# Kernel optimization log

Measured on AMD Instinct MI355X. Metric: run time of the kernel, lower is better.

## Reference

```python
import jax, jax.numpy as jnp
import numpy as np

K_UNF = 11   # unfold kernel = 15 - 4
PAD = 1      # reflection padding for attention branch
KC = 5       # ConvBlock kernel_conv
HEADS = 4
CIN = 64
HD = CIN // HEADS  # head_dim = 16
EPS = 1e-5


def _unfold(x, k):
    # x: [b,C,H,W] -> [b, C*k*k, oh*ow] with torch.nn.Unfold ordering (c, kh, kw)
    b, C, H, W = x.shape
    oh, ow = H - k + 1, W - k + 1
    ih = jnp.arange(oh)[:, None] + jnp.arange(k)[None, :]  # [oh,k]
    iw = jnp.arange(ow)[:, None] + jnp.arange(k)[None, :]  # [ow,k]
    p = x[:, :, ih, :]          # [b,C,oh,k,W]
    p = p[:, :, :, :, iw]       # [b,C,oh,k,ow,k]
    p = p.transpose(0, 1, 3, 5, 2, 4)  # [b,C,kh,kw,oh,ow]
    return p.reshape(b, C * k * k, oh * ow)


def _bn_train(x):
    # BatchNorm2d in training mode, weight=1, bias=0 (fresh module defaults)
    m = x.mean(axis=(0, 2, 3), keepdims=True)
    v = x.var(axis=(0, 2, 3), keepdims=True)
    return (x - m) * jax.lax.rsqrt(v + EPS)


def setup_inputs() -> dict:
    key = jax.random.key(0)
    ks = jax.random.split(key, 6)
    b = 64
    s = 0.02
    x1 = jax.random.normal(ks[0], (b, CIN, 15, 15), jnp.float32)
    Wq = jax.random.normal(ks[1], (CIN, CIN), jnp.float32) * s
    Wk = jax.random.normal(ks[2], (CIN, CIN), jnp.float32) * s
    Wv = jax.random.normal(ks[3], (CIN, CIN), jnp.float32) * s
    fc_w = jax.random.normal(ks[4], (KC * KC, 3 * HEADS), jnp.float32) * s
    convg_w = jax.random.normal(ks[5], (CIN, CIN, 3, 3), jnp.float32) * s
    # dep_conv weight: deterministic one-hot shift kernels per reset_parameters
    dk = np.zeros((KC * KC, KC, KC), np.float32)
    for i in range(KC * KC):
        dk[i, i // KC, i % KC] = 1.0
    dep_w = jnp.asarray(np.broadcast_to(dk[None], (CIN, KC * KC, KC, KC)).copy())
    return {"x1": x1, "Wq": Wq, "Wk": Wk, "Wv": Wv, "fc_w": fc_w,
            "dep_w": dep_w, "convg_w": convg_w}


def reference(x1, Wq, Wk, Wv, fc_w, dep_w, convg_w):
    b, C, h, w = x1.shape  # h=w=15 (i=1 -> size=15)
    size = h
    # 1x1 qkv convs
    q = jnp.einsum('oc,bchw->bohw', Wq, x1)
    k = jnp.einsum('oc,bchw->bohw', Wk, x1)
    v = jnp.einsum('oc,bchw->bohw', Wv, x1)
    # ---- conv branch (ConvBlock) ----
    qkv = jnp.concatenate([t.reshape(b, HEADS, HD, h * w) for t in (q, k, v)], axis=1)  # [b,12,16,225]
    f_all = jnp.einsum('oc,bcds->bods', fc_w, qkv)                 # [b,25,16,225]
    f_conv = f_all.transpose(0, 2, 1, 3).reshape(b, HD * KC * KC, h, w)  # [b,400,15,15]
    out_conv = jax.lax.conv_general_dilated(
        f_conv, dep_w, (1, 1), 'VALID',
        dimension_numbers=('NCHW', 'OIHW', 'NCHW'),
        feature_group_count=HD)                                     # [b,64,11,11]; bias is None
    out_conv = _bn_train(out_conv)
    # ---- attention branch (UnfoldBlock + raw scaled QK^T, no softmax) ----
    def pad_unfold(t):
        tp = jnp.pad(t, ((0, 0), (0, 0), (PAD, PAD), (PAD, PAD)), mode='reflect')
        u = _unfold(tp, K_UNF).transpose(0, 2, 1)  # [b,49,7744]; pos_embed is zeros
        cls = jnp.zeros((b, 1, u.shape[-1]), u.dtype)  # cls token params are zeros
        return jnp.concatenate([cls, u], axis=1)       # [b,50,7744]
    uq, uk, uv = pad_unfold(q), pad_unfold(k), pad_unfold(v)
    N, Cq = uq.shape[1], uq.shape[2]
    query = uq.reshape(b, HEADS, N, Cq // HEADS)  # matches torch reshape semantics
    key_ = uk.reshape(b, HEADS, N, Cq // HEADS)
    val = uv.reshape(b, HEADS, N, Cq // HEADS)
    scaling = float(HD) ** -0.5
    att = jnp.einsum('bhnc,bhmc->bhnm', query, key_) * scaling   # [b,4,50,50]
    out_attn = jnp.einsum('bhnm,bhmc->bhnc', att, val)
    out_attn = out_attn.transpose(0, 2, 1, 3).reshape(b, N, Cq)
    out_attn = out_attn[:, 1, :].reshape(b, CIN, size - 4, size - 4)  # [b,64,11,11]
    out_attn = jax.lax.conv_general_dilated(
        out_attn, convg_w, (1, 1), ((1, 1), (1, 1)),
        dimension_numbers=('NCHW', 'OIHW', 'NCHW'))
    # rate1 and rate2 are filled with 0.5 every forward
    return out_conv * 0.5 + out_attn * 0.5
```

## Files before the change

### kernel.cpp

```cpp
#include <hip/hip_runtime.h>
#include <hip/hip_bf16.h>

#define B 64
#define CIN 64
#define HW 225
#define CQ 7744
#define XS2 116
#define VPS 24

__device__ __forceinline__ int reflect15(int t) {
    return t < 0 ? -t : (t > 14 ? 28 - t : t);
}
__device__ __forceinline__ int refp(int t) { return reflect15(t - 1); }

__global__ __launch_bounds__(512) void qkv_kernel(const float* __restrict__ x1,
                           const float* __restrict__ Wq,
                           const float* __restrict__ Wk,
                           const float* __restrict__ Wv,
                           float* __restrict__ q, float* __restrict__ k, float* __restrict__ v,
                           float* __restrict__ stats) {
    int b = blockIdx.x;
    int t = blockIdx.y;
    int ph = blockIdx.z;
    int tid = threadIdx.x;
    if (b == 0 && t == 0 && ph == 0 && tid < 32) stats[tid] = 0.f;
    const float* W = (t == 0) ? Wq : (t == 1) ? Wk : Wv;
    float* out = (t == 0) ? q : (t == 1) ? k : v;
    __shared__ float xs[CIN * XS2];
    int start = ph ? 113 : 0;
    int count = ph ? 112 : 113;
    const float* xb = x1 + (size_t)b * CIN * HW;
    for (int i = tid; i < CIN * XS2; i += 512) {
        int c = i / XS2, s = i % XS2;
        xs[i] = (s < count) ? xb[c * HW + start + s] : 0.f;
    }
    __syncthreads();
    int og = __builtin_amdgcn_readfirstlane(tid >> 6);
    int lane = tid & 63;
    const float* Wb = W + (size_t)og * 8 * CIN;
    float acc[8][2];
    #pragma unroll
    for (int m = 0; m < 8; ++m) { acc[m][0] = 0.f; acc[m][1] = 0.f; }
    #pragma unroll 4
    for (int c = 0; c < CIN; ++c) {
        float x0 = xs[c * XS2 + lane];
        float x1v = xs[c * XS2 + lane + 64];
        #pragma unroll
        for (int m = 0; m < 8; ++m) {
            float w = Wb[m * CIN + c];
            acc[m][0] += w * x0;
            acc[m][1] += w * x1v;
        }
    }
    float* ob = out + (size_t)b * CIN * HW;
    #pragma unroll
    for (int m = 0; m < 8; ++m) {
        int o = og * 8 + m;
        #pragma unroll
        for (int j = 0; j < 2; ++j) {
            int s = lane + 64 * j;
            if (s < count) ob[o * HW + start + s] = acc[m][j];
        }
    }
}

__global__ void conv5_kernel(const float* __restrict__ q, const float* __restrict__ k,
                             const float* __restrict__ v, const float* __restrict__ fc_w,
                             float* __restrict__ ocpre, float* __restrict__ stats) {
    int b = blockIdx.x, g = blockIdx.y;
    __shared__ float chs[12][HW];
    __shared__ float red[128], red2[128];
    const float* srcs[3] = {q, k, v};
    for (int i = threadIdx.x; i < 12 * HW; i += blockDim.x) {
        int c = i / HW, s = i % HW;
        int t = c >> 2, hd = c & 3;
        chs[c][s] = srcs[t][(size_t)b * CIN * HW + (hd * 16 + g) * HW + s];
    }
    __syncthreads();
    float myval = 0.f;
    int yx = threadIdx.x;
    if (yx < 121) {
        int y = yx / 11, x = yx % 11;
        float acc = 0.f;
        #pragma unroll
        for (int c = 0; c < 12; ++c) {
            #pragma unroll
            for (int kh = 0; kh < 5; ++kh) {
                #pragma unroll
                for (int kw = 0; kw < 5; ++kw) {
                    acc += fc_w[(kh * 5 + kw) * 12 + c] * chs[c][(y + kh) * 15 + (x + kw)];
                }
            }
        }
        ocpre[((size_t)b * 16 + g) * 121 + yx] = acc;
        myval = acc;
    }
    red[threadIdx.x] = myval;
    red2[threadIdx.x] = myval * myval;
    __syncthreads();
    for (int s = 64; s > 0; s >>= 1) {
        if (threadIdx.x < s) {
            red[threadIdx.x] += red[threadIdx.x + s];
            red2[threadIdx.x] += red2[threadIdx.x + s];
        }
        __syncthreads();
    }
    if (threadIdx.x == 0) {
        atomicAdd(&stats[g], red[0]);
        atomicAdd(&stats[16 + g], red2[0]);
    }
}

__global__ void qk_kernel(const float* __restrict__ q, const float* __restrict__ k,
                          float* __restrict__ att_g) {
    int b = blockIdx.x, hh = blockIdx.y, qq = blockIdx.z;
    __shared__ float kp[16 * 289];
    __shared__ float qw[16 * 121];
    int tid = threadIdx.x;
    const float* kb = k + ((size_t)b * CIN + qq * 16) * HW;
    for (int i = tid; i < 16 * 289; i += 256) {
        int ch = i / 289, rr = i % 289;
        int yy = rr / 17, xx = rr % 17;
        kp[i] = kb[ch * HW + refp(yy) * 15 + refp(xx)];
    }
    {
        int gq = 50 * hh + 1;
        int rq = gq >> 2;
        if (rq == 0) {
            for (int i = tid; i < 16 * 121; i += 256) qw[i] = 0.f;
        } else {
            int cq = (gq & 3) * 16;
            int p = rq - 1, py0 = p / 7, px0 = p % 7;
            const float* qb = q + ((size_t)b * CIN + cq) * HW;
            for (int i = tid; i < 16 * 121; i += 256) {
                int cl = i / 121, rr = i % 121;
                int ki = rr / 11, kj = rr % 11;
                qw[i] = qb[cl * HW + refp(py0 + ki) * 15 + refp(px0 + kj)];
            }
        }
    }
    __syncthreads();
    int wave = tid >> 6, lane = tid & 63;
    int m0 = (qq - 2 * hh) & 3;
    int nt = (50 - m0 + 3) >> 2;
    float* ag = att_g + ((size_t)b * 4 + hh) * 64;
    for (int t = wave; t < nt; t += 4) {
        int m = m0 + t * 4;
        int g = 50 * hh + m;
        int r = g >> 2;
        float acc = 0.f;
        if (r > 0) {
            int p = r - 1, py = p / 7, px = p % 7;
            #pragma unroll
            for (int it = 0; it < 3; ++it) {
                int rw = lane + it * 64;
                if (rw < 176) {
                    int cl = rw / 11, ki = rw % 11;
                    const float* kr = kp + cl * 289 + (py + ki) * 17 + px;
                    const float* qr = qw + cl * 121 + ki * 11;
                    float s = 0.f;
                    #pragma unroll
                    for (int kj = 0; kj < 11; ++kj) s += qr[kj] * kr[kj];
                    acc += s;
                }
            }
            #pragma unroll
            for (int off = 32; off > 0; off >>= 1) acc += __shfl_xor(acc, off);
        }
        if (lane == 0) ag[m] = acc * 0.25f;
    }
}

__global__ __launch_bounds__(512) void pv_kernel(const float* __restrict__ v,
                          const float* __restrict__ att_g,
                          float* __restrict__ attn_img) {
    int b = blockIdx.x, hh = blockIdx.y;
    __shared__ float vp[64 * 17 * VPS];
    __shared__ float am[4 * 49];
    int tid = threadIdx.x;
    const float* vb = v + (size_t)b * CIN * HW;
    for (int i = tid; i < 64 * 17 * VPS; i += 512) {
        int ch = i / (17 * VPS), rr = i % (17 * VPS);
        int yy = rr / VPS, xx = rr % VPS;
        vp[i] = (xx < 17) ? vb[ch * HW + refp(yy) * 15 + refp(xx)] : 0.f;
    }
    if (tid < 196) am[tid] = 0.f;
    __syncthreads();
    if (tid < 50) {
        int g = 50 * hh + tid;
        int r = g >> 2;
        if (r > 0) am[(g & 3) * 49 + (r - 1)] = att_g[((size_t)b * 4 + hh) * 64 + tid];
    }
    __syncthreads();
    int lane = tid & 63;
    int w = tid;
    int cl = w / 22, rem = w % 22;
    int y = rem >> 1, xh = rem & 1;
    int x0 = xh * 8;
    int nx = xh ? 3 : 8;
    bool act = w < 352;
    float acc[8] = {0, 0, 0, 0, 0, 0, 0, 0};
    #pragma unroll
    for (int qq = 0; qq < 4; ++qq) {
        float amv = 0.f;
        if (lane < 49) amv = am[qq * 49 + lane];
        if (act) {
            const float* base = vp + (qq * 16 + cl) * (17 * VPS);
            #pragma unroll
            for (int py = 0; py < 7; ++py) {
                const float* row = base + (y + py) * VPS + x0;
                float4 r0 = *(const float4*)(row);
                float4 r1 = *(const float4*)(row + 4);
                float4 r2 = *(const float4*)(row + 8);
                float4 r3 = *(const float4*)(row + 12);
                float rv[16] = {r0.x, r0.y, r0.z, r0.w, r1.x, r1.y, r1.z, r1.w,
                                r2.x, r2.y, r2.z, r2.w, r3.x, r3.y, r3.z, r3.w};
                #pragma unroll
                for (int px = 0; px < 7; ++px) {
                    float a = __uint_as_float(
                        __builtin_amdgcn_readlane(__float_as_uint(amv), py * 7 + px));
                    #pragma unroll
                    for (int i = 0; i < 8; ++i) acc[i] += a * rv[px + i];
                }
            }
        }
    }
    if (act) {
        float* outp = attn_img + (size_t)b * CQ + hh * 1936 + cl * 121 + y * 11 + x0;
        for (int i = 0; i < nx; ++i) outp[i] = acc[i];
    }
}

__global__ __launch_bounds__(512, 2) void final_kernel(
                             const float* __restrict__ ocpre, const float* __restrict__ stats,
                             const float* __restrict__ attn_img, const float* __restrict__ convg_w,
                             float* __restrict__ out) {
    int b = blockIdx.x, og = blockIdx.y;
    __shared__ float ap[CIN * 169];
    __shared__ float red[3 * 8 * 128];
    int tid = threadIdx.x;
    for (int i = tid; i < CIN * 169; i += 512) ap[i] = 0.f;
    __syncthreads();
    for (int i = tid; i < CIN * 121; i += 512) {
        int c = i / 121, ss = i % 121;
        ap[c * 169 + (ss / 11 + 1) * 13 + (ss % 11 + 1)] = attn_img[(size_t)b * CQ + i];
    }
    __syncthreads();
    int qu = __builtin_amdgcn_readfirstlane(tid >> 7);
    int slot = tid & 127;
    int px = slot < 121 ? slot : 120;
    int y = px / 11, x = px % 11;
    float f0 = 0.f, f1 = 0.f, f2 = 0.f, f3 = 0.f, f4 = 0.f, f5 = 0.f, f6 = 0.f, f7 = 0.f;
    const float* wb = convg_w + ((size_t)og * 8 * CIN + qu * 16) * 9;
    for (int c16 = 0; c16 < 16; ++c16) {
        const float* apc = ap + (qu * 16 + c16) * 169 + y * 13 + x;
        float a00 = apc[0],  a01 = apc[1],  a02 = apc[2];
        float a10 = apc[13], a11 = apc[14], a12 = apc[15];
        float a20 = apc[26], a21 = apc[27], a22 = apc[28];
        #pragma unroll
        for (int oo = 0; oo < 8; ++oo) {
            const float* w = wb + (oo * CIN + c16) * 9;
            float s = w[0] * a00 + w[1] * a01 + w[2] * a02
                    + w[3] * a10 + w[4] * a11 + w[5] * a12
                    + w[6] * a20 + w[7] * a21 + w[8] * a22;
            switch (oo) {
                case 0: f0 += s; break; case 1: f1 += s; break;
                case 2: f2 += s; break; case 3: f3 += s; break;
                case 4: f4 += s; break; case 5: f5 += s; break;
                case 6: f6 += s; break; case 7: f7 += s; break;
            }
        }
    }
    if (qu > 0) {
        float* r = red + (qu - 1) * 1024 + slot;
        r[0 * 128] = f0; r[1 * 128] = f1; r[2 * 128] = f2; r[3 * 128] = f3;
        r[4 * 128] = f4; r[5 * 128] = f5; r[6 * 128] = f6; r[7 * 128] = f7;
    }
    __syncthreads();
    if (qu == 0 && slot < 121) {
        #pragma unroll
        for (int qq = 0; qq < 3; ++qq) {
            const float* r = red + qq * 1024 + slot;
            f0 += r[0 * 128]; f1 += r[1 * 128]; f2 += r[2 * 128]; f3 += r[3 * 128];
            f4 += r[4 * 128]; f5 += r[5 * 128]; f6 += r[6 * 128]; f7 += r[7 * 128];
        }
        int g0 = og * 2, g1 = og * 2 + 1;
        float m0 = stats[g0] * (1.f / 7744.f);
        float m1 = stats[g1] * (1.f / 7744.f);
        float v0 = stats[16 + g0] * (1.f / 7744.f) - m0 * m0;
        float v1 = stats[16 + g1] * (1.f / 7744.f) - m1 * m1;
        float r0 = rsqrtf(v0 + 1e-5f);
        float r1 = rsqrtf(v1 + 1e-5f);
        float bn0 = (ocpre[((size_t)b * 16 + g0) * 121 + slot] - m0) * r0;
        float bn1 = (ocpre[((size_t)b * 16 + g1) * 121 + slot] - m1) * r1;
        float* ob = out + ((size_t)b * CIN + og * 8) * 121 + slot;
        ob[0 * 121] = 0.5f * bn0 + 0.5f * f0;
        ob[1 * 121] = 0.5f * bn0 + 0.5f * f1;
        ob[2 * 121] = 0.5f * bn0 + 0.5f * f2;
        ob[3 * 121] = 0.5f * bn0 + 0.5f * f3;
        ob[4 * 121] = 0.5f * bn1 + 0.5f * f4;
        ob[5 * 121] = 0.5f * bn1 + 0.5f * f5;
        ob[6 * 121] = 0.5f * bn1 + 0.5f * f6;
        ob[7 * 121] = 0.5f * bn1 + 0.5f * f7;
    }
}

extern "C" void kernel_launch(void* const* d_in, const int* in_sizes, int n_in,
                              void* d_out, int out_size, void* d_ws, size_t ws_size,
                              hipStream_t stream) {
    const float* x1     = (const float*)d_in[0];
    const float* Wq     = (const float*)d_in[1];
    const float* Wk     = (const float*)d_in[2];
    const float* Wv     = (const float*)d_in[3];
    const float* fc_w   = (const float*)d_in[4];
    const float* convg_w = (const float*)d_in[6];
    float* out = (float*)d_out;

    char* ws = (char*)d_ws;
    float* q        = (float*)(ws);
    float* k        = (float*)(ws + 3686400);
    float* v        = (float*)(ws + 7372800);
    float* ocpre    = (float*)(ws + 11059200);
    float* stats    = (float*)(ws + 11554816);
    float* attn_img = (float*)(ws + 11555072);
    float* att_g    = (float*)(ws + 13537536);

    hipLaunchKernelGGL(qkv_kernel, dim3(64, 3, 2), dim3(512), 0, stream, x1, Wq, Wk, Wv, q, k, v, stats);
    hipLaunchKernelGGL(conv5_kernel, dim3(64, 16), dim3(128), 0, stream, q, k, v, fc_w, ocpre, stats);
    hipLaunchKernelGGL(qk_kernel, dim3(64, 4, 4), dim3(256), 0, stream, q, k, att_g);
    hipLaunchKernelGGL(pv_kernel, dim3(64, 4), dim3(512), 0, stream, v, att_g, attn_img);
    hipLaunchKernelGGL(final_kernel, dim3(64, 8), dim3(512), 0, stream, ocpre, stats, attn_img, convg_w, out);
}
```

Baseline: 169.8 us.

## Merge conv5 and qk kernels into one launch; split pv_kernel over channel halves

The conv-branch 5x5 kernel and the QK attention-score kernel are merged into one mid_kernel. Block role selects the work: roles 0-7 compute two conv groups each, roles 8-23 compute QK scores. This removes a kernel launch and lets the two independent stages share the GPU. pv_kernel is split along a new grid z dimension into two channel halves with 256 threads and half the shared memory, giving twice as many smaller blocks for better occupancy. The cost is that pv now loads the attention matrix redundantly per half, and mid_kernel mixes heterogeneous blocks that may finish unevenly.

New measurement: 157.6 us. 7.2% less time.

```diff
diff --git a/kernel.cpp b/kernel.cpp
--- a/kernel.cpp
+++ b/kernel.cpp
@@ -64,123 +64,135 @@
     }
 }
 
-__global__ void conv5_kernel(const float* __restrict__ q, const float* __restrict__ k,
-                             const float* __restrict__ v, const float* __restrict__ fc_w,
-                             float* __restrict__ ocpre, float* __restrict__ stats) {
-    int b = blockIdx.x, g = blockIdx.y;
-    __shared__ float chs[12][HW];
-    __shared__ float red[128], red2[128];
-    const float* srcs[3] = {q, k, v};
-    for (int i = threadIdx.x; i < 12 * HW; i += blockDim.x) {
-        int c = i / HW, s = i % HW;
-        int t = c >> 2, hd = c & 3;
-        chs[c][s] = srcs[t][(size_t)b * CIN * HW + (hd * 16 + g) * HW + s];
-    }
-    __syncthreads();
-    float myval = 0.f;
-    int yx = threadIdx.x;
-    if (yx < 121) {
-        int y = yx / 11, x = yx % 11;
-        float acc = 0.f;
-        #pragma unroll
-        for (int c = 0; c < 12; ++c) {
+__global__ __launch_bounds__(256) void mid_kernel(const float* __restrict__ q,
+                           const float* __restrict__ k, const float* __restrict__ v,
+                           const float* __restrict__ fc_w,
+                           float* __restrict__ ocpre, float* __restrict__ stats,
+                           float* __restrict__ att_g) {
+    __shared__ float smem[16 * 289 + 16 * 121];
+    int b = blockIdx.x, role = blockIdx.y;
+    int tid = threadIdx.x;
+    if (role < 8) {
+        int g0 = role * 2, g1 = role * 2 + 1;
+        float* chs = smem;
+        float* red = smem + 5400;
+        float* red2 = smem + 5656;
+        const float* srcs[3] = {q, k, v};
+        for (int i = tid; i < 24 * HW; i += 256) {
+            int c = i / HW, s = i % HW;
+            int half = c / 12, cc = c % 12;
+            int t = cc >> 2, hd = cc & 3;
+            int g = half ? g1 : g0;
+            chs[c * HW + s] = srcs[t][(size_t)b * CIN * HW + (hd * 16 + g) * HW + s];
+        }
+        __syncthreads();
+        int h = tid >> 7;
+        int yx = tid & 127;
+        float myval = 0.f;
+        if (yx < 121) {
+            int y = yx / 11, x = yx % 11;
+            const float* ch0 = chs + h * 12 * HW;
+            float acc = 0.f;
             #pragma unroll
-            for (int kh = 0; kh < 5; ++kh) {
+            for (int c = 0; c < 12; ++c) {
                 #pragma unroll
-                for (int kw = 0; kw < 5; ++kw) {
-                    acc += fc_w[(kh * 5 + kw) * 12 + c] * chs[c][(y + kh) * 15 + (x + kw)];
+                for (int kh = 0; kh < 5; ++kh) {
+                    #pragma unroll
+                    for (int kw = 0; kw < 5; ++kw) {
+                        acc += fc_w[(kh * 5 + kw) * 12 + c] * ch0[c * HW + (y + kh) * 15 + (x + kw)];
+                    }
                 }
             }
-        }
-        ocpre[((size_t)b * 16 + g) * 121 + yx] = acc;
-        myval = acc;
-    }
-    red[threadIdx.x] = myval;
-    red2[threadIdx.x] = myval * myval;
-    __syncthreads();
-    for (int s = 64; s > 0; s >>= 1) {
-        if (threadIdx.x < s) {
-            red[threadIdx.x] += red[threadIdx.x + s];
-            red2[threadIdx.x] += red2[threadIdx.x + s];
-        }
+            ocpre[((size_t)b * 16 + (h ? g1 : g0)) * 121 + yx] = acc;
+            myval = acc;
+        }
+        red[tid] = myval;
+        red2[tid] = myval * myval;
         __syncthreads();
-    }
-    if (threadIdx.x == 0) {
-        atomicAdd(&stats[g], red[0]);
-        atomicAdd(&stats[16 + g], red2[0]);
-    }
-}
-
-__global__ void qk_kernel(const float* __restrict__ q, const float* __restrict__ k,
-                          float* __restrict__ att_g) {
-    int b = blockIdx.x, hh = blockIdx.y, qq = blockIdx.z;
-    __shared__ float kp[16 * 289];
-    __shared__ float qw[16 * 121];
-    int tid = threadIdx.x;
-    const float* kb = k + ((size_t)b * CIN + qq * 16) * HW;
-    for (int i = tid; i < 16 * 289; i += 256) {
-        int ch = i / 289, rr = i % 289;
-        int yy = rr / 17, xx = rr % 17;
-        kp[i] = kb[ch * HW + refp(yy) * 15 + refp(xx)];
-    }
-    {
-        int gq = 50 * hh + 1;
-        int rq = gq >> 2;
-        if (rq == 0) {
-            for (int i = tid; i < 16 * 121; i += 256) qw[i] = 0.f;
-        } else {
-            int cq = (gq & 3) * 16;
-            int p = rq - 1, py0 = p / 7, px0 = p % 7;
-            const float* qb = q + ((size_t)b * CIN + cq) * HW;
-            for (int i = tid; i < 16 * 121; i += 256) {
-                int cl = i / 121, rr = i % 121;
-                int ki = rr / 11, kj = rr % 11;
-                qw[i] = qb[cl * HW + refp(py0 + ki) * 15 + refp(px0 + kj)];
-            }
-        }
-    }
-    __syncthreads();
-    int wave = tid >> 6, lane = tid & 63;
-    int m0 = (qq - 2 * hh) & 3;
-    int nt = (50 - m0 + 3) >> 2;
-    float* ag = att_g + ((size_t)b * 4 + hh) * 64;
-    for (int t = wave; t < nt; t += 4) {
-        int m = m0 + t * 4;
-        int g = 50 * hh + m;
-        int r = g >> 2;
-        float acc = 0.f;
-        if (r > 0) {
-            int p = r - 1, py = p / 7, px = p % 7;
-            #pragma unroll
-            for (int it = 0; it < 3; ++it) {
-                int rw = lane + it * 64;
-                if (rw < 176) {
-                    int cl = rw / 11, ki = rw % 11;
-                    const float* kr = kp + cl * 289 + (py + ki) * 17 + px;
-                    const float* qr = qw + cl * 121 + ki * 11;
-                    float s = 0.f;
-                    #pragma unroll
-                    for (int kj = 0; kj < 11; ++kj) s += qr[kj] * kr[kj];
-                    acc += s;
+        for (int s = 64; s > 0; s >>= 1) {
+            if ((tid & 127) < s) {
+                red[tid] += red[tid + s];
+                red2[tid] += red2[tid + s];
+            }
+            __syncthreads();
+        }
+        if ((tid & 127) == 0) {
+            int g = (tid >> 7) ? g1 : g0;
+            atomicAdd(&stats[g], red[tid]);
+            atomicAdd(&stats[16 + g], red2[tid]);
+        }
+    } else {
+        int idx = role - 8;
+        int hh = idx >> 2, qq = idx & 3;
+        float* kp = smem;
+        float* qw = smem + 16 * 289;
+        const float* kb = k + ((size_t)b * CIN + qq * 16) * HW;
+        for (int i = tid; i < 16 * 289; i += 256) {
+            int ch = i / 289, rr = i % 289;
+            int yy = rr / 17, xx = rr % 17;
+            kp[i] = kb[ch * HW + refp(yy) * 15 + refp(xx)];
+        }
+        {
+            int gq = 50 * hh + 1;
+            int rq = gq >> 2;
+            if (rq == 0) {
+                for (int i = tid; i < 16 * 121; i += 256) qw[i] = 0.f;
+            } else {
+                int cq = (gq & 3) * 16;
+                int p = rq - 1, py0 = p / 7, px0 = p % 7;
+                const float* qb = q + ((size_t)b * CIN + cq) * HW;
+                for (int i = tid; i < 16 * 121; i += 256) {
+                    int cl = i / 121, rr = i % 121;
+                    int ki = rr / 11, kj = rr % 11;
+                    qw[i] = qb[cl * HW + refp(py0 + ki) * 15 + refp(px0 + kj)];
                 }
             }
-            #pragma unroll
-            for (int off = 32; off > 0; off >>= 1) acc += __shfl_xor(acc, off);
-        }
-        if (lane == 0) ag[m] = acc * 0.25f;
-    }
-}
-
-__global__ __launch_bounds__(512) void pv_kernel(const float* __restrict__ v,
+        }
+        __syncthreads();
+        int wave = tid >> 6, lane = tid & 63;
+        int m0 = (qq - 2 * hh) & 3;
+        int nt = (50 - m0 + 3) >> 2;
+        float* ag = att_g + ((size_t)b * 4 + hh) * 64;
+        for (int t = wave; t < nt; t += 4) {
+            int m = m0 + t * 4;
+            int g = 50 * hh + m;
+            int r = g >> 2;
+            float acc = 0.f;
+            if (r > 0) {
+                int p = r - 1, py = p / 7, px = p % 7;
+                #pragma unroll
+                for (int it = 0; it < 3; ++it) {
+                    int rw = lane + it * 64;
+                    if (rw < 176) {
+                        int cl = rw / 11, ki = rw % 11;
+                        const float* kr = kp + cl * 289 + (py + ki) * 17 + px;
+                        const float* qr = qw + cl * 121 + ki * 11;
+                        float s = 0.f;
+                        #pragma unroll
+                        for (int kj = 0; kj < 11; ++kj) s += qr[kj] * kr[kj];
+                        acc += s;
+                    }
+                }
+                #pragma unroll
+                for (int off = 32; off > 0; off >>= 1) acc += __shfl_xor(acc, off);
+            }
+            if (lane == 0) ag[m] = acc * 0.25f;
+        }
+    }
+}
+
+__global__ __launch_bounds__(256) void pv_kernel(const float* __restrict__ v,
                           const float* __restrict__ att_g,
                           float* __restrict__ attn_img) {
-    int b = blockIdx.x, hh = blockIdx.y;
-    __shared__ float vp[64 * 17 * VPS];
+    int b = blockIdx.x, hh = blockIdx.y, z = blockIdx.z;
+    __shared__ float vp[32 * 17 * VPS];
     __shared__ float am[4 * 49];
     int tid = threadIdx.x;
     const float* vb = v + (size_t)b * CIN * HW;
-    for (int i = tid; i < 64 * 17 * VPS; i += 512) {
-        int ch = i / (17 * VPS), rr = i % (17 * VPS);
+    for (int i = tid; i < 32 * 17 * VPS; i += 256) {
+        int idx = i / (17 * VPS), rr = i % (17 * VPS);
+        int qq = idx >> 3, cls = idx & 7;
+        int ch = qq * 16 + z * 8 + cls;
         int yy = rr / VPS, xx = rr % VPS;
         vp[i] = (xx < 17) ? vb[ch * HW + refp(yy) * 15 + refp(xx)] : 0.f;
     }
@@ -194,18 +206,18 @@
     __syncthreads();
     int lane = tid & 63;
     int w = tid;
-    int cl = w / 22, rem = w % 22;
+    int cls = w / 22, rem = w % 22;
     int y = rem >> 1, xh = rem & 1;
     int x0 = xh * 8;
     int nx = xh ? 3 : 8;
-    bool act = w < 352;
+    bool act = w < 176;
     float acc[8] = {0, 0, 0, 0, 0, 0, 0, 0};
     #pragma unroll
     for (int qq = 0; qq < 4; ++qq) {
         float amv = 0.f;
         if (lane < 49) amv = am[qq * 49 + lane];
         if (act) {
-            const float* base = vp + (qq * 16 + cl) * (17 * VPS);
+            const float* base = vp + (qq * 8 + cls) * (17 * VPS);
             #pragma unroll
             for (int py = 0; py < 7; ++py) {
                 const float* row = base + (y + py) * VPS + x0;
@@ -226,7 +238,7 @@
         }
     }
     if (act) {
-        float* outp = attn_img + (size_t)b * CQ + hh * 1936 + cl * 121 + y * 11 + x0;
+        float* outp = attn_img + (size_t)b * CQ + hh * 1936 + (z * 8 + cls) * 121 + y * 11 + x0;
         for (int i = 0; i < nx; ++i) outp[i] = acc[i];
     }
 }
@@ -326,8 +338,7 @@
     float* att_g    = (float*)(ws + 13537536);
 
     hipLaunchKernelGGL(qkv_kernel, dim3(64, 3, 2), dim3(512), 0, stream, x1, Wq, Wk, Wv, q, k, v, stats);
-    hipLaunchKernelGGL(conv5_kernel, dim3(64, 16), dim3(128), 0, stream, q, k, v, fc_w, ocpre, stats);
-    hipLaunchKernelGGL(qk_kernel, dim3(64, 4, 4), dim3(256), 0, stream, q, k, att_g);
-    hipLaunchKernelGGL(pv_kernel, dim3(64, 4), dim3(512), 0, stream, v, att_g, attn_img);
+    hipLaunchKernelGGL(mid_kernel, dim3(64, 24), dim3(256), 0, stream, q, k, v, fc_w, ocpre, stats, att_g);
+    hipLaunchKernelGGL(pv_kernel, dim3(64, 4, 2), dim3(256), 0, stream, v, att_g, attn_img);
     hipLaunchKernelGGL(final_kernel, dim3(64, 8), dim3(512), 0, stream, ocpre, stats, attn_img, convg_w, out);
 }
```

## Fuse conv5, QK and PV stages into one per-batch mega kernel

Applied to the files above, without the earlier changes.

Merges the conv-branch kernel, the attention-score kernel and the attention-value kernel into one 1024-thread block per (batch, head pair). K is staged once in shared memory and shared by the conv branch and the QK product. Attention weights stay in shared memory rather than making a round trip through global memory. BatchNorm stats are written as per-batch partials and summed in the final kernel, replacing global atomics and the zeroing step. This removes two launches and intermediate traffic, but the grid shrinks to 128 large blocks with heavy LDS use, so occupancy and parallelism drop.

New measurement: 164.0 us. -3.4%, faster.

```diff
diff --git a/kernel.cpp b/kernel.cpp
--- a/kernel.cpp
+++ b/kernel.cpp
@@ -6,7 +6,10 @@
 #define HW 225
 #define CQ 7744
 #define XS2 116
-#define VPS 24
+#define KPS 21
+#define KPCH 357
+#define VXS 20
+#define VXCH 300
 
 __device__ __forceinline__ int reflect15(int t) {
     return t < 0 ? -t : (t > 14 ? 28 - t : t);
@@ -17,13 +20,11 @@
                            const float* __restrict__ Wq,
                            const float* __restrict__ Wk,
                            const float* __restrict__ Wv,
-                           float* __restrict__ q, float* __restrict__ k, float* __restrict__ v,
-                           float* __restrict__ stats) {
+                           float* __restrict__ q, float* __restrict__ k, float* __restrict__ v) {
     int b = blockIdx.x;
     int t = blockIdx.y;
     int ph = blockIdx.z;
     int tid = threadIdx.x;
-    if (b == 0 && t == 0 && ph == 0 && tid < 32) stats[tid] = 0.f;
     const float* W = (t == 0) ? Wq : (t == 1) ? Wk : Wv;
     float* out = (t == 0) ? q : (t == 1) ? k : v;
     __shared__ float xs[CIN * XS2];
@@ -64,175 +65,174 @@
     }
 }
 
-__global__ void conv5_kernel(const float* __restrict__ q, const float* __restrict__ k,
-                             const float* __restrict__ v, const float* __restrict__ fc_w,
-                             float* __restrict__ ocpre, float* __restrict__ stats) {
-    int b = blockIdx.x, g = blockIdx.y;
-    __shared__ float chs[12][HW];
-    __shared__ float red[128], red2[128];
-    const float* srcs[3] = {q, k, v};
-    for (int i = threadIdx.x; i < 12 * HW; i += blockDim.x) {
-        int c = i / HW, s = i % HW;
-        int t = c >> 2, hd = c & 3;
-        chs[c][s] = srcs[t][(size_t)b * CIN * HW + (hd * 16 + g) * HW + s];
-    }
-    __syncthreads();
-    float myval = 0.f;
-    int yx = threadIdx.x;
-    if (yx < 121) {
-        int y = yx / 11, x = yx % 11;
-        float acc = 0.f;
-        #pragma unroll
-        for (int c = 0; c < 12; ++c) {
-            #pragma unroll
-            for (int kh = 0; kh < 5; ++kh) {
-                #pragma unroll
-                for (int kw = 0; kw < 5; ++kw) {
-                    acc += fc_w[(kh * 5 + kw) * 12 + c] * chs[c][(y + kh) * 15 + (x + kw)];
-                }
-            }
-        }
-        ocpre[((size_t)b * 16 + g) * 121 + yx] = acc;
-        myval = acc;
-    }
-    red[threadIdx.x] = myval;
-    red2[threadIdx.x] = myval * myval;
-    __syncthreads();
-    for (int s = 64; s > 0; s >>= 1) {
-        if (threadIdx.x < s) {
-            red[threadIdx.x] += red[threadIdx.x + s];
-            red2[threadIdx.x] += red2[threadIdx.x + s];
-        }
-        __syncthreads();
-    }
-    if (threadIdx.x == 0) {
-        atomicAdd(&stats[g], red[0]);
-        atomicAdd(&stats[16 + g], red2[0]);
-    }
-}
-
-__global__ void qk_kernel(const float* __restrict__ q, const float* __restrict__ k,
-                          float* __restrict__ att_g) {
-    int b = blockIdx.x, hh = blockIdx.y, qq = blockIdx.z;
-    __shared__ float kp[16 * 289];
-    __shared__ float qw[16 * 121];
+__global__ __launch_bounds__(1024) void mega_kernel(
+        const float* __restrict__ q, const float* __restrict__ k, const float* __restrict__ v,
+        const float* __restrict__ fc_w,
+        float* __restrict__ ocpre, float* __restrict__ stats_part,
+        float* __restrict__ attn_img) {
+    int b = blockIdx.x, hz = blockIdx.y;
     int tid = threadIdx.x;
-    const float* kb = k + ((size_t)b * CIN + qq * 16) * HW;
-    for (int i = tid; i < 16 * 289; i += 256) {
+    __shared__ float buf[26720];
+    __shared__ float amb[2 * 4 * 49];
+    float* kp = buf;
+    float* qw = buf + 22848;
+
+    const float* kb = k + (size_t)b * CIN * HW;
+    for (int i = tid; i < 64 * 289; i += 1024) {
         int ch = i / 289, rr = i % 289;
         int yy = rr / 17, xx = rr % 17;
-        kp[i] = kb[ch * HW + refp(yy) * 15 + refp(xx)];
-    }
-    {
-        int gq = 50 * hh + 1;
-        int rq = gq >> 2;
-        if (rq == 0) {
-            for (int i = tid; i < 16 * 121; i += 256) qw[i] = 0.f;
-        } else {
+        kp[ch * KPCH + yy * KPS + xx] = kb[ch * HW + refp(yy) * 15 + refp(xx)];
+    }
+    for (int i = tid; i < 2 * 16 * 121; i += 1024) {
+        int clg = i / 121, r = i % 121;
+        int hhl = clg >> 4, cl = clg & 15;
+        int hh = 2 * hz + hhl;
+        int gq = 50 * hh + 1, rq = gq >> 2;
+        float val = 0.f;
+        if (rq > 0) {
             int cq = (gq & 3) * 16;
             int p = rq - 1, py0 = p / 7, px0 = p % 7;
-            const float* qb = q + ((size_t)b * CIN + cq) * HW;
-            for (int i = tid; i < 16 * 121; i += 256) {
-                int cl = i / 121, rr = i % 121;
-                int ki = rr / 11, kj = rr % 11;
-                qw[i] = qb[cl * HW + refp(py0 + ki) * 15 + refp(px0 + kj)];
+            int ki = r / 11, kj = r % 11;
+            val = q[((size_t)b * CIN + cq + cl) * HW + refp(py0 + ki) * 15 + refp(px0 + kj)];
+        }
+        qw[i] = val;
+    }
+    if (tid < 392) amb[tid] = 0.f;
+    __syncthreads();
+
+    int w = tid >> 6, lane = tid & 63;
+    if (w < 8) {
+        int g = hz * 8 + w;
+        float vsum = 0.f, vsq = 0.f;
+        #pragma unroll
+        for (int half = 0; half < 2; ++half) {
+            int px = lane + 64 * half;
+            float acc = 0.f;
+            if (px < 121) {
+                int y = px / 11, x = px % 11;
+                #pragma unroll
+                for (int c = 0; c < 12; ++c) {
+                    int t = c >> 2, hd = c & 3;
+                    int ch = hd * 16 + g;
+                    if (t == 1) {
+                        const float* kc = kp + ch * KPCH;
+                        #pragma unroll
+                        for (int kh = 0; kh < 5; ++kh)
+                            #pragma unroll
+                            for (int kw = 0; kw < 5; ++kw)
+                                acc += fc_w[(kh * 5 + kw) * 12 + c] * kc[(y + kh + 1) * KPS + x + kw + 1];
+                    } else {
+                        const float* sc = ((t == 0) ? q : v) + ((size_t)b * CIN + ch) * HW;
+                        #pragma unroll
+                        for (int kh = 0; kh < 5; ++kh)
+                            #pragma unroll
+                            for (int kw = 0; kw < 5; ++kw)
+                                acc += fc_w[(kh * 5 + kw) * 12 + c] * sc[(y + kh) * 15 + x + kw];
+                    }
+                }
+                ocpre[((size_t)b * 16 + g) * 121 + px] = acc;
             }
-        }
-    }
-    __syncthreads();
-    int wave = tid >> 6, lane = tid & 63;
-    int m0 = (qq - 2 * hh) & 3;
-    int nt = (50 - m0 + 3) >> 2;
-    float* ag = att_g + ((size_t)b * 4 + hh) * 64;
-    for (int t = wave; t < nt; t += 4) {
-        int m = m0 + t * 4;
-        int g = 50 * hh + m;
-        int r = g >> 2;
-        float acc = 0.f;
-        if (r > 0) {
+            vsum += acc; vsq += acc * acc;
+        }
+        #pragma unroll
+        for (int off = 32; off > 0; off >>= 1) {
+            vsum += __shfl_xor(vsum, off);
+            vsq  += __shfl_xor(vsq, off);
+        }
+        if (lane == 0) {
+            stats_part[b * 32 + g] = vsum;
+            stats_part[b * 32 + 16 + g] = vsq;
+        }
+    } else {
+        int idx = w - 8;
+        int hhl = idx >> 2, qq = idx & 3;
+        int hh = 2 * hz + hhl;
+        float qr[3][11];
+        int rb[3];
+        #pragma unroll
+        for (int it = 0; it < 3; ++it) {
+            int rw = lane + it * 64;
+            bool ok = rw < 176;
+            int cl = ok ? rw / 11 : 0;
+            int ki = ok ? rw % 11 : 0;
+            rb[it] = (qq * 16 + cl) * KPCH + ki * KPS;
+            const float* qrp = qw + (hhl * 16 + cl) * 121 + ki * 11;
+            #pragma unroll
+            for (int kj = 0; kj < 11; ++kj) qr[it][kj] = ok ? qrp[kj] : 0.f;
+        }
+        int m0 = (qq - 2 * hh) & 3;
+        for (int m = m0; m < 50; m += 4) {
+            int g = 50 * hh + m;
+            int r = g >> 2;
+            if (r == 0) continue;
             int p = r - 1, py = p / 7, px = p % 7;
+            int aoff = py * KPS + px;
+            float acc = 0.f;
             #pragma unroll
             for (int it = 0; it < 3; ++it) {
-                int rw = lane + it * 64;
-                if (rw < 176) {
-                    int cl = rw / 11, ki = rw % 11;
-                    const float* kr = kp + cl * 289 + (py + ki) * 17 + px;
-                    const float* qr = qw + cl * 121 + ki * 11;
-                    float s = 0.f;
-                    #pragma unroll
-                    for (int kj = 0; kj < 11; ++kj) s += qr[kj] * kr[kj];
-                    acc += s;
-                }
+                const float* kr = kp + rb[it] + aoff;
+                #pragma unroll
+                for (int kj = 0; kj < 11; ++kj) acc += qr[it][kj] * kr[kj];
             }
             #pragma unroll
             for (int off = 32; off > 0; off >>= 1) acc += __shfl_xor(acc, off);
-        }
-        if (lane == 0) ag[m] = acc * 0.25f;
-    }
-}
-
-__global__ __launch_bounds__(512) void pv_kernel(const float* __restrict__ v,
-                          const float* __restrict__ att_g,
-                          float* __restrict__ attn_img) {
-    int b = blockIdx.x, hh = blockIdx.y;
-    __shared__ float vp[64 * 17 * VPS];
-    __shared__ float am[4 * 49];
-    int tid = threadIdx.x;
+            if (lane == 0) amb[(hhl * 4 + qq) * 49 + p] = acc * 0.25f;
+        }
+    }
+    __syncthreads();
+
+    float* Vx = buf;
     const float* vb = v + (size_t)b * CIN * HW;
-    for (int i = tid; i < 64 * 17 * VPS; i += 512) {
-        int ch = i / (17 * VPS), rr = i % (17 * VPS);
-        int yy = rr / VPS, xx = rr % VPS;
-        vp[i] = (xx < 17) ? vb[ch * HW + refp(yy) * 15 + refp(xx)] : 0.f;
-    }
-    if (tid < 196) am[tid] = 0.f;
-    __syncthreads();
-    if (tid < 50) {
-        int g = 50 * hh + tid;
-        int r = g >> 2;
-        if (r > 0) am[(g & 3) * 49 + (r - 1)] = att_g[((size_t)b * 4 + hh) * 64 + tid];
-    }
-    __syncthreads();
-    int lane = tid & 63;
-    int w = tid;
-    int cl = w / 22, rem = w % 22;
-    int y = rem >> 1, xh = rem & 1;
-    int x0 = xh * 8;
-    int nx = xh ? 3 : 8;
-    bool act = w < 352;
-    float acc[8] = {0, 0, 0, 0, 0, 0, 0, 0};
-    #pragma unroll
-    for (int qq = 0; qq < 4; ++qq) {
-        float amv = 0.f;
-        if (lane < 49) amv = am[qq * 49 + lane];
-        if (act) {
-            const float* base = vp + (qq * 16 + cl) * (17 * VPS);
-            #pragma unroll
-            for (int py = 0; py < 7; ++py) {
-                const float* row = base + (y + py) * VPS + x0;
-                float4 r0 = *(const float4*)(row);
-                float4 r1 = *(const float4*)(row + 4);
-                float4 r2 = *(const float4*)(row + 8);
-                float4 r3 = *(const float4*)(row + 12);
-                float rv[16] = {r0.x, r0.y, r0.z, r0.w, r1.x, r1.y, r1.z, r1.w,
-                                r2.x, r2.y, r2.z, r2.w, r3.x, r3.y, r3.z, r3.w};
+    for (int i = tid; i < 64 * VXCH; i += 1024) {
+        int ch = i / VXCH, rr = i % VXCH;
+        int y = rr / VXS, xx = rr % VXS;
+        Vx[i] = (xx < 17) ? vb[ch * HW + y * 15 + refp(xx)] : 0.f;
+    }
+    if (tid < 8) Vx[64 * VXCH + tid] = 0.f;
+    __syncthreads();
+    {
+        int hhl = tid >> 9;
+        int rem = tid & 511;
+        int hh = 2 * hz + hhl;
+        int cl = rem / 22, r2 = rem % 22;
+        int y = r2 >> 1, xh = r2 & 1;
+        int x0 = xh * 8;
+        int nx = xh ? 3 : 8;
+        bool act = rem < 352;
+        float acc[8] = {0, 0, 0, 0, 0, 0, 0, 0};
+        #pragma unroll
+        for (int qq = 0; qq < 4; ++qq) {
+            float amv = (lane < 49) ? amb[hhl * 196 + qq * 49 + lane] : 0.f;
+            if (act) {
+                const float* base = Vx + (qq * 16 + cl) * VXCH;
                 #pragma unroll
-                for (int px = 0; px < 7; ++px) {
-                    float a = __uint_as_float(
-                        __builtin_amdgcn_readlane(__float_as_uint(amv), py * 7 + px));
+                for (int py = 0; py < 7; ++py) {
+                    const float* row = base + refp(y + py) * VXS + x0;
+                    float4 r0 = *(const float4*)(row);
+                    float4 r1 = *(const float4*)(row + 4);
+                    float4 r2v = *(const float4*)(row + 8);
+                    float4 r3 = *(const float4*)(row + 12);
+                    float rv[16] = {r0.x, r0.y, r0.z, r0.w, r1.x, r1.y, r1.z, r1.w,
+                                    r2v.x, r2v.y, r2v.z, r2v.w, r3.x, r3.y, r3.z, r3.w};
                     #pragma unroll
-                    for (int i = 0; i < 8; ++i) acc[i] += a * rv[px + i];
+                    for (int px = 0; px < 7; ++px) {
+                        float a = __uint_as_float(
+                            __builtin_amdgcn_readlane(__float_as_uint(amv), py * 7 + px));
+                        #pragma unroll
+                        for (int i = 0; i < 8; ++i) acc[i] += a * rv[px + i];
+                    }
                 }
             }
         }
-    }
-    if (act) {
-        float* outp = attn_img + (size_t)b * CQ + hh * 1936 + cl * 121 + y * 11 + x0;
-        for (int i = 0; i < nx; ++i) outp[i] = acc[i];
+        if (act) {
+            float* outp = attn_img + (size_t)b * CQ + hh * 1936 + cl * 121 + y * 11 + x0;
+            for (int i = 0; i < nx; ++i) outp[i] = acc[i];
+        }
     }
 }
 
 __global__ __launch_bounds__(512, 2) void final_kernel(
-                             const float* __restrict__ ocpre, const float* __restrict__ stats,
+                             const float* __restrict__ ocpre, const float* __restrict__ stats_part,
                              const float* __restrict__ attn_img, const float* __restrict__ convg_w,
                              float* __restrict__ out) {
     int b = blockIdx.x, og = blockIdx.y;
@@ -285,10 +285,16 @@
             f4 += r[4 * 128]; f5 += r[5 * 128]; f6 += r[6 * 128]; f7 += r[7 * 128];
         }
         int g0 = og * 2, g1 = og * 2 + 1;
-        float m0 = stats[g0] * (1.f / 7744.f);
-        float m1 = stats[g1] * (1.f / 7744.f);
-        float v0 = stats[16 + g0] * (1.f / 7744.f) - m0 * m0;
-        float v1 = stats[16 + g1] * (1.f / 7744.f) - m1 * m1;
+        float su0 = 0.f, sq0 = 0.f, su1 = 0.f, sq1 = 0.f;
+        for (int bb = 0; bb < 64; ++bb) {
+            const float* sp = stats_part + bb * 32;
+            su0 += sp[g0]; sq0 += sp[16 + g0];
+            su1 += sp[g1]; sq1 += sp[16 + g1];
+        }
+        float m0 = su0 * (1.f / 7744.f);
+        float m1 = su1 * (1.f / 7744.f);
+        float v0 = sq0 * (1.f / 7744.f) - m0 * m0;
+        float v1 = sq1 * (1.f / 7744.f) - m1 * m1;
         float r0 = rsqrtf(v0 + 1e-5f);
         float r1 = rsqrtf(v1 + 1e-5f);
         float bn0 = (ocpre[((size_t)b * 16 + g0) * 121 + slot] - m0) * r0;
@@ -317,17 +323,14 @@
     float* out = (float*)d_out;
 
     char* ws = (char*)d_ws;
-    float* q        = (float*)(ws);
-    float* k        = (float*)(ws + 3686400);
-    float* v        = (float*)(ws + 7372800);
-    float* ocpre    = (float*)(ws + 11059200);
-    float* stats    = (float*)(ws + 11554816);
-    float* attn_img = (float*)(ws + 11555072);
-    float* att_g    = (float*)(ws + 13537536);
-
-    hipLaunchKernelGGL(qkv_kernel, dim3(64, 3, 2), dim3(512), 0, stream, x1, Wq, Wk, Wv, q, k, v, stats);
-    hipLaunchKernelGGL(conv5_kernel, dim3(64, 16), dim3(128), 0, stream, q, k, v, fc_w, ocpre, stats);
-    hipLaunchKernelGGL(qk_kernel, dim3(64, 4, 4), dim3(256), 0, stream, q, k, att_g);
-    hipLaunchKernelGGL(pv_kernel, dim3(64, 4), dim3(512), 0, stream, v, att_g, attn_img);
-    hipLaunchKernelGGL(final_kernel, dim3(64, 8), dim3(512), 0, stream, ocpre, stats, attn_img, convg_w, out);
-}
+    float* q          = (float*)(ws);
+    float* k          = (float*)(ws + 3686400);
+    float* v          = (float*)(ws + 7372800);
+    float* ocpre      = (float*)(ws + 11059200);
+    float* stats_part = (float*)(ws + 11554816);
+    float* attn_img   = (float*)(ws + 11563008);
+
+    hipLaunchKernelGGL(qkv_kernel, dim3(64, 3, 2), dim3(512), 0, stream, x1, Wq, Wk, Wv, q, k, v);
+    hipLaunchKernelGGL(mega_kernel, dim3(64, 2), dim3(1024), 0, stream, q, k, v, fc_w, ocpre, stats_part, attn_img);
+    hipLaunchKernelGGL(final_kernel, dim3(64, 8), dim3(512), 0, stream, ocpre, stats_part, attn_img, convg_w, out);
+}
```
